# Optimization experiments

Hardware: AMD Instinct MI355X
Metric: run time of the kernel (lower is better)

The kernel has to match this reference:

```python
import jax, jax.numpy as jnp
import numpy as np

N, H, W = 32, 1024, 1024

# fixed 2x2 stencil kernel [[1, .5], [.5, .25]] applied after zero-padding
# one row at the bottom and one column at the right (so output keeps HxW):
#   out[i, j] = x[i, j] + .5*x[i, j+1] + .5*x[i+1, j] + .25*x[i+1, j+1]

def _stencil(x):
    # x: [N, H, W] -> [N, H, W]
    p = jnp.pad(x, ((0, 0), (0, 1), (0, 1)))
    return (p[:, :-1, :-1]
            + 0.5 * p[:, :-1, 1:]
            + 0.5 * p[:, 1:, :-1]
            + 0.25 * p[:, 1:, 1:])


def setup_inputs() -> dict:
    key = jax.random.key(0)
    img = jax.random.normal(key, (N, H, W), dtype=jnp.float32)
    return {"img": img}


def reference(img):
    y = _stencil(img)
    y = y[::-1]          # torch.flip(dims=[0]) on [N,1,H,W] -> batch reversal
    y = _stencil(y)      # torch.flip(dims=[1]) flips size-1 channel dim: no-op
    y = _stencil(y)
    y = y[::-1]          # second batch reversal
    y = _stencil(y)      # final channel flip is again a no-op
    return y
```

## Files before the change

kernel.cpp:

```cpp
#include <hip/hip_runtime.h>


#define N_IMG 32
#define H_IMG 1024
#define W_IMG 1024
#define RPT 8

__global__ __launch_bounds__(256) void stencil4_kernel(const float* __restrict__ in,
                                                       float* __restrict__ out) {
    const float c0 = 1.0f, c1 = 2.0f, c2 = 1.5f, c3 = 0.5f, c4 = 0.0625f;

    const int j0 = threadIdx.x * 4;
    const int i0 = blockIdx.x * RPT;
    const int n  = blockIdx.y;

    const float* img = in  + (size_t)n * H_IMG * W_IMG;
    float*       o   = out + (size_t)n * H_IMG * W_IMG;

    float4 f[RPT + 4];

    #pragma unroll
    for (int r = 0; r < RPT + 4; ++r) {
        const int i = i0 + r;
        float4 a = make_float4(0.f, 0.f, 0.f, 0.f);
        float4 b = make_float4(0.f, 0.f, 0.f, 0.f);
        if (i < H_IMG) {
            a = *reinterpret_cast<const float4*>(img + (size_t)i * W_IMG + j0);
            if (j0 + 4 < W_IMG) {
                b = *reinterpret_cast<const float4*>(img + (size_t)i * W_IMG + j0 + 4);
            }
        }
        float4 t;
        t.x = c0*a.x + c1*a.y + c2*a.z + c3*a.w + c4*b.x;
        t.y = c0*a.y + c1*a.z + c2*a.w + c3*b.x + c4*b.y;
        t.z = c0*a.z + c1*a.w + c2*b.x + c3*b.y + c4*b.z;
        t.w = c0*a.w + c1*b.x + c2*b.y + c3*b.z + c4*b.w;
        f[r] = t;
    }

    #pragma unroll
    for (int r = 0; r < RPT; ++r) {
        float4 y;
        y.x = c0*f[r].x + c1*f[r+1].x + c2*f[r+2].x + c3*f[r+3].x + c4*f[r+4].x;
        y.y = c0*f[r].y + c1*f[r+1].y + c2*f[r+2].y + c3*f[r+3].y + c4*f[r+4].y;
        y.z = c0*f[r].z + c1*f[r+1].z + c2*f[r+2].z + c3*f[r+3].z + c4*f[r+4].z;
        y.w = c0*f[r].w + c1*f[r+1].w + c2*f[r+2].w + c3*f[r+3].w + c4*f[r+4].w;
        *reinterpret_cast<float4*>(o + (size_t)(i0 + r) * W_IMG + j0) = y;
    }
}

extern "C" void kernel_launch(void* const* d_in, const int* in_sizes, int n_in,
                              void* d_out, int out_size, void* d_ws, size_t ws_size,
                              hipStream_t stream) {
    const float* img = (const float*)d_in[0];
    float*       out = (float*)d_out;

    dim3 grid(H_IMG / RPT, N_IMG);
    dim3 block(256);
    stencil4_kernel<<<grid, block, 0, stream>>>(img, out);
}
```

Baseline: 262.9 us.

## Stage input rows in LDS via direct global-to-LDS loads with split wait

Replaces the per-thread double float4 global loads with global_load_lds instructions that stream the 12 input rows straight into a padded shared-memory tile. The horizontal filter then reads its neighbour columns from LDS instead of issuing a second overlapping global load. A partial vmcnt wait lets the first four output rows be computed while the last four row loads are still in flight. The cost is LDS usage and barriers, which may lower occupancy, plus hand-written waitcnt assembly whose counting must match the compiler's instruction order.

```diff
diff --git a/kernel.cpp b/kernel.cpp
--- a/kernel.cpp
+++ b/kernel.cpp
@@ -4,48 +4,99 @@
 #define N_IMG 32
 #define H_IMG 1024
 #define W_IMG 1024
-#define RPT 8
+#define R_OUT 8
+#define NROWS (R_OUT + 4)
+#define ROWF  (W_IMG + 8)
+#define ROWB  (ROWF * 4)
 
-__global__ __launch_bounds__(256) void stencil4_kernel(const float* __restrict__ in,
-                                                       float* __restrict__ out) {
+#define GLOAD16(gp, lp) __builtin_amdgcn_global_load_lds(                     \
+    (const __attribute__((address_space(1))) void*)(gp),                      \
+    (__attribute__((address_space(3))) void*)(lp), 16, 0, 0)
+
+__device__ __forceinline__ float4 rowfilt(const float* __restrict__ row) {
     const float c0 = 1.0f, c1 = 2.0f, c2 = 1.5f, c3 = 0.5f, c4 = 0.0625f;
+    float4 a = *reinterpret_cast<const float4*>(row);
+    float4 b = *reinterpret_cast<const float4*>(row + 4);
+    float4 t;
+    t.x = c0*a.x + c1*a.y + c2*a.z + c3*a.w + c4*b.x;
+    t.y = c0*a.y + c1*a.z + c2*a.w + c3*b.x + c4*b.y;
+    t.z = c0*a.z + c1*a.w + c2*b.x + c3*b.y + c4*b.z;
+    t.w = c0*a.w + c1*b.x + c2*b.y + c3*b.z + c4*b.w;
+    return t;
+}
 
-    const int j0 = threadIdx.x * 4;
-    const int i0 = blockIdx.x * RPT;
-    const int n  = blockIdx.y;
+__device__ __forceinline__ float4 colcomb(float4 w0, float4 w1, float4 w2,
+                                          float4 w3, float4 t) {
+    const float c0 = 1.0f, c1 = 2.0f, c2 = 1.5f, c3 = 0.5f, c4 = 0.0625f;
+    float4 y;
+    y.x = c0*w0.x + c1*w1.x + c2*w2.x + c3*w3.x + c4*t.x;
+    y.y = c0*w0.y + c1*w1.y + c2*w2.y + c3*w3.y + c4*t.y;
+    y.z = c0*w0.z + c1*w1.z + c2*w2.z + c3*w3.z + c4*t.z;
+    y.w = c0*w0.w + c1*w1.w + c2*w2.w + c3*w3.w + c4*t.w;
+    return y;
+}
 
+__global__ __launch_bounds__(256) void stencil4_lds(const float* __restrict__ in,
+                                                    float* __restrict__ out) {
+    __shared__ float tile[NROWS * ROWF];
+
+    const int tid = threadIdx.x;
+    const int i0  = blockIdx.x * R_OUT;
+    const int n   = blockIdx.y;
     const float* img = in  + (size_t)n * H_IMG * W_IMG;
     float*       o   = out + (size_t)n * H_IMG * W_IMG;
 
-    float4 f[RPT + 4];
+    if (tid < NROWS * 2) {
+        int q = tid >> 1, s = tid & 1;
+        *reinterpret_cast<float4*>(&tile[q * ROWF + W_IMG + s * 4]) =
+            make_float4(0.f, 0.f, 0.f, 0.f);
+    }
+    #pragma unroll
+    for (int q = R_OUT; q < NROWS; ++q) {
+        if (i0 + q >= H_IMG) {
+            *reinterpret_cast<float4*>(&tile[q * ROWF + tid * 4]) =
+                make_float4(0.f, 0.f, 0.f, 0.f);
+        }
+    }
+
+    const int wave_byte = (tid >> 6) * 1024;
+    const int lane_col  = (tid & 63) * 4 + (tid >> 6) * 256;
+    #pragma unroll
+    for (int q = 0; q < NROWS; ++q) {
+        if (i0 + q < H_IMG) {
+            GLOAD16(img + (size_t)(i0 + q) * W_IMG + lane_col,
+                    (char*)tile + q * ROWB + wave_byte);
+        }
+    }
+
+    if (i0 + NROWS - 1 < H_IMG) {
+        asm volatile("s_waitcnt vmcnt(4) lgkmcnt(0)\n\ts_barrier" ::: "memory");
+    } else {
+        asm volatile("s_waitcnt vmcnt(0) lgkmcnt(0)\n\ts_barrier" ::: "memory");
+    }
+
+    const int j0 = tid * 4;
+    float4 w0 = rowfilt(&tile[0 * ROWF + j0]);
+    float4 w1 = rowfilt(&tile[1 * ROWF + j0]);
+    float4 w2 = rowfilt(&tile[2 * ROWF + j0]);
+    float4 w3 = rowfilt(&tile[3 * ROWF + j0]);
 
     #pragma unroll
-    for (int r = 0; r < RPT + 4; ++r) {
-        const int i = i0 + r;
-        float4 a = make_float4(0.f, 0.f, 0.f, 0.f);
-        float4 b = make_float4(0.f, 0.f, 0.f, 0.f);
-        if (i < H_IMG) {
-            a = *reinterpret_cast<const float4*>(img + (size_t)i * W_IMG + j0);
-            if (j0 + 4 < W_IMG) {
-                b = *reinterpret_cast<const float4*>(img + (size_t)i * W_IMG + j0 + 4);
-            }
-        }
-        float4 t;
-        t.x = c0*a.x + c1*a.y + c2*a.z + c3*a.w + c4*b.x;
-        t.y = c0*a.y + c1*a.z + c2*a.w + c3*b.x + c4*b.y;
-        t.z = c0*a.z + c1*a.w + c2*b.x + c3*b.y + c4*b.z;
-        t.w = c0*a.w + c1*b.x + c2*b.y + c3*b.z + c4*b.w;
-        f[r] = t;
+    for (int r = 0; r < 4; ++r) {
+        float4 t = rowfilt(&tile[(r + 4) * ROWF + j0]);
+        float4 y = colcomb(w0, w1, w2, w3, t);
+        *reinterpret_cast<float4*>(o + (size_t)(i0 + r) * W_IMG + j0) = y;
+        w0 = w1; w1 = w2; w2 = w3; w3 = t;
     }
 
+    asm volatile("s_waitcnt vmcnt(0) lgkmcnt(0)\n\ts_barrier" ::: "memory");
+
     #pragma unroll
-    for (int r = 0; r < RPT; ++r) {
-        float4 y;
-        y.x = c0*f[r].x + c1*f[r+1].x + c2*f[r+2].x + c3*f[r+3].x + c4*f[r+4].x;
-        y.y = c0*f[r].y + c1*f[r+1].y + c2*f[r+2].y + c3*f[r+3].y + c4*f[r+4].y;
-        y.z = c0*f[r].z + c1*f[r+1].z + c2*f[r+2].z + c3*f[r+3].z + c4*f[r+4].z;
-        y.w = c0*f[r].w + c1*f[r+1].w + c2*f[r+2].w + c3*f[r+3].w + c4*f[r+4].w;
+    for (int r = 4; r < R_OUT; ++r) {
+        float4 t = rowfilt(&tile[(r + 4) * ROWF + j0]);
+        float4 y = colcomb(w0, w1, w2, w3, t);
         *reinterpret_cast<float4*>(o + (size_t)(i0 + r) * W_IMG + j0) = y;
+        w0 = w1; w1 = w2; w2 = w3; w3 = t;
     }
 }
 
@@ -55,7 +106,7 @@
     const float* img = (const float*)d_in[0];
     float*       out = (float*)d_out;
 
-    dim3 grid(H_IMG / RPT, N_IMG);
+    dim3 grid(H_IMG / R_OUT, N_IMG);
     dim3 block(256);
-    stencil4_kernel<<<grid, block, 0, stream>>>(img, out);
+    stencil4_lds<<<grid, block, 0, stream>>>(img, out);
 }
```

Result: faster. 229.2 us (-12.8%).
